# Performance work log

Hardware: AMD Instinct MI355X
Metric: run time of the kernel (lower is better)

The kernel has to match this reference:

```python
import jax, jax.numpy as jnp
import numpy as np
from jax import lax

# Mamba2 config (matches init_kwargs + mamba_ssm defaults)
B_SZ, SEQ = 8, 2048
D_MODEL, D_STATE, EXPAND, HEADDIM = 1024, 128, 2, 64
D_INNER = EXPAND * D_MODEL            # 2048
NHEADS = D_INNER // HEADDIM           # 32
NGROUPS, D_CONV, CHUNK = 1, 4, 128
CONV_DIM = D_INNER + 2 * NGROUPS * D_STATE
D_IN_PROJ = 2 * D_INNER + 2 * NGROUPS * D_STATE + NHEADS
VAR_NUM, EPS = 3, 1e-5


def setup_inputs() -> dict:
    key = jax.random.key(0)
    ks = jax.random.split(key, 10)
    return {
        "embed_data": jax.random.normal(ks[0], (B_SZ, SEQ, D_MODEL), jnp.float32),
        "in_proj_w": jax.random.normal(ks[1], (D_IN_PROJ, D_MODEL), jnp.float32) * 0.02,
        "conv_w": jax.random.normal(ks[2], (CONV_DIM, D_CONV), jnp.float32) * 0.2,
        "conv_b": jnp.zeros((CONV_DIM,), jnp.float32),
        "dt_bias": jnp.log(jnp.expm1(jax.random.uniform(ks[3], (NHEADS,), jnp.float32, 1e-3, 0.1))),
        "A_log": jnp.log(jax.random.uniform(ks[4], (NHEADS,), jnp.float32, 1.0, 16.0)),
        "D": jnp.ones((NHEADS,), jnp.float32),
        "norm_w": jnp.ones((D_INNER,), jnp.float32),
        "out_proj_w": jax.random.normal(ks[5], (D_MODEL, D_INNER), jnp.float32) * 0.02,
        "dec_w": jax.random.normal(ks[6], (VAR_NUM, D_MODEL), jnp.float32) * 0.02,
        "dec_b": jnp.zeros((VAR_NUM,), jnp.float32),
    }


def _segsum(a):
    # a: (b,h,c,L) -> (b,h,c,L,L) lower-triangular segment sums
    L = a.shape[-1]
    cs = jnp.cumsum(a, -1)
    ss = cs[..., :, None] - cs[..., None, :]
    mask = jnp.tril(jnp.ones((L, L), bool))
    return jnp.where(mask, ss, -jnp.inf)


def _ssd(x, dt, A, Bm, Cm):
    # x:(b,l,h,p) dt:(b,l,h) A:(h,) Bm,Cm:(b,l,n); chunked SSD scan (Mamba2)
    b, l, h, p = x.shape
    n = Bm.shape[-1]
    c = l // CHUNK
    xc = x.reshape(b, c, CHUNK, h, p)
    dtc = dt.reshape(b, c, CHUNK, h)
    Bc = Bm.reshape(b, c, CHUNK, n)
    Cc = Cm.reshape(b, c, CHUNK, n)
    ac = (dt * A).reshape(b, c, CHUNK, h).transpose(0, 3, 1, 2)  # (b,h,c,L)
    acs = jnp.cumsum(ac, -1)
    Lmat = jnp.exp(_segsum(ac))                                   # (b,h,c,L,L)
    xdt = xc * dtc[..., None]
    # intra-chunk (diagonal block) outputs
    CB = jnp.einsum('bcln,bcsn->bcls', Cc, Bc)
    Y_diag = jnp.einsum('bcls,bhcls,bcshp->bclhp', CB, Lmat, xdt)
    # per-chunk final states
    decay_states = jnp.exp(acs[..., -1:] - acs)                   # (b,h,c,L)
    states = jnp.einsum('bcln,bhcl,bclhp->bchpn', Bc, decay_states, xdt)
    chunk_decay = jnp.exp(acs[..., -1])                           # (b,h,c)
    def step(carry, inp):
        st, dec = inp
        return carry * dec[..., None, None] + st, carry
    _, states_in = lax.scan(step, jnp.zeros((b, h, p, n), x.dtype),
                            (jnp.moveaxis(states, 1, 0), jnp.moveaxis(chunk_decay, 2, 0)))
    states_in = jnp.moveaxis(states_in, 0, 1)                     # (b,c,h,p,n)
    # inter-chunk (off-diagonal) contribution
    Y_off = jnp.einsum('bcln,bchpn,bhcl->bclhp', Cc, states_in, jnp.exp(acs))
    return (Y_diag + Y_off).reshape(b, l, h, p)


def reference(embed_data, in_proj_w, conv_w, conv_b, dt_bias, A_log, D, norm_w, out_proj_w, dec_w, dec_b):
    b, l, _ = embed_data.shape
    zxbcdt = embed_data @ in_proj_w.T                             # (b,l,D_IN_PROJ)
    z = zxbcdt[..., :D_INNER]
    xBC = zxbcdt[..., D_INNER:D_INNER + CONV_DIM]
    dt = jax.nn.softplus(zxbcdt[..., D_INNER + CONV_DIM:] + dt_bias)  # (b,l,h)
    # causal depthwise conv1d + SiLU
    xt = lax.conv_general_dilated(xBC.transpose(0, 2, 1), conv_w[:, None, :], (1,),
                                  [(D_CONV - 1, 0)], feature_group_count=CONV_DIM,
                                  dimension_numbers=('NCH', 'OIH', 'NCH'))
    xBC = jax.nn.silu(xt.transpose(0, 2, 1) + conv_b)
    x = xBC[..., :D_INNER].reshape(b, l, NHEADS, HEADDIM)
    Bm = xBC[..., D_INNER:D_INNER + D_STATE]
    Cm = xBC[..., D_INNER + D_STATE:]
    A = -jnp.exp(A_log)
    y = _ssd(x, dt, A, Bm, Cm) + D[None, None, :, None] * x
    # gated RMSNorm
    y = y.reshape(b, l, D_INNER) * jax.nn.silu(z)
    y = y * lax.rsqrt(jnp.mean(y * y, -1, keepdims=True) + EPS) * norm_w
    hidden = y @ out_proj_w.T
    pred = hidden @ dec_w.T + dec_b
    return pred, hidden
```

## Files before the change

kernel.cpp:

```cpp
#include <hip/hip_runtime.h>
#include <cstdint>

#define DEVI __device__ __forceinline__

typedef unsigned short u16;
typedef unsigned int u32;
typedef __attribute__((ext_vector_type(4))) float f32x4;
typedef __attribute__((ext_vector_type(8))) u16 u16x8;
typedef __attribute__((ext_vector_type(4))) u16 u16x4;
typedef __attribute__((ext_vector_type(8))) __bf16 bf16x8;

#define SEQL 2048
#define NBATCH 8
#define MROWS (NBATCH*SEQL)
#define DMODEL 1024
#define DINNER 2048
#define NHEADS 32
#define HEADD 64
#define DSTATE 128
#define CONVD 2304
#define NPROJ 4384
#define NPROJP 4608
#define CHUNKL 128
#define NCHUNK 16
#define PADC 136

DEVI float bf2f(u16 v){ u32 u = ((u32)v)<<16; return __builtin_bit_cast(float,u); }
DEVI u16 f2bf(float f){ u32 u = __builtin_bit_cast(u32,f); u32 r = (u + 0x7fffu + ((u>>16)&1u))>>16; return (u16)r; }

DEVI void gld_lds16(const void* g, void* lds){
  __builtin_amdgcn_global_load_lds(
    (const __attribute__((address_space(1))) void*)(uintptr_t)g,
    (__attribute__((address_space(3))) void*)(u32)(uintptr_t)lds, 16, 0, 0);
}

DEVI f32x4 MFMA(u16x8 a, u16x8 b, f32x4 c){
  return __builtin_amdgcn_mfma_f32_16x16x32_bf16(
      __builtin_bit_cast(bf16x8,a), __builtin_bit_cast(bf16x8,b), c, 0,0,0);
}

__global__ void k_sentinel(float* o){ o[0] = 12345.0f; }

__global__ __launch_bounds__(256) void k_cvt(const float* __restrict__ src, u16* __restrict__ dst, long n, long ntot){
  long idx = ((long)blockIdx.x*256 + threadIdx.x)*4;
  if (idx >= ntot) return;
  u16x4 o;
  if (idx < n){
    f32x4 v = *(const f32x4*)(src+idx);
    o[0]=f2bf(v[0]); o[1]=f2bf(v[1]); o[2]=f2bf(v[2]); o[3]=f2bf(v[3]);
  } else { o[0]=0; o[1]=0; o[2]=0; o[3]=0; }
  *(u16x4*)(dst+idx) = o;
}

#define STG(mat, h, ts) do { \
    const int d_ = (ts) & 1; \
    const size_t ko_ = (size_t)(((ts) < NT) ? (ts) : (NT-1)) * 64; \
    gld_lds16(sbase[mat][h][0] + ko_, (char*)lds + (mat)*65536 + (d_*2+(h))*16384 + tid*16); \
    gld_lds16(sbase[mat][h][1] + ko_, (char*)lds + (mat)*65536 + (d_*2+(h))*16384 + 8192 + tid*16); \
  } while(0)

#define LDA8(AF, d_, qm) { \
    _Pragma("unroll") for (int mf=0; mf<4; mf++) \
    _Pragma("unroll") for (int ks=0; ks<2; ks++) \
      AF[mf][ks] = *(const u16x8*)(lds + (size_t)((d_)*2+wm)*8192 + ((qm)*64+mf*16+lidx)*64 + ((ks*4+krow)^(lidx&7))*8); }

#define LDB4(BF, d_, qn) { \
    _Pragma("unroll") for (int nf=0; nf<2; nf++) \
    _Pragma("unroll") for (int ks=0; ks<2; ks++) \
      BF[nf][ks] = *(const u16x8*)(lds + 32768 + (size_t)((d_)*2+(wn>>1))*8192 + ((wn&1)*64+(qn)*32+nf*16+lidx)*64 + ((ks*4+krow)^(lidx&7))*8); }

#define MMAQ(QM, QN, AF, BF) { \
    _Pragma("unroll") for (int mf=0; mf<4; mf++) \
    _Pragma("unroll") for (int nf=0; nf<2; nf++) \
    _Pragma("unroll") for (int ks=0; ks<2; ks++) \
      acc[(QM)*4+mf][(QN)*2+nf] = MFMA(AF[mf][ks], BF[nf][ks], acc[(QM)*4+mf][(QN)*2+nf]); }

#define BAR1 __builtin_amdgcn_sched_barrier(0); __builtin_amdgcn_s_barrier(); \
    asm volatile("s_waitcnt lgkmcnt(0)" ::: "memory"); __builtin_amdgcn_sched_barrier(0); \
    __builtin_amdgcn_s_setprio(1);
#define BAR2 __builtin_amdgcn_s_setprio(0); __builtin_amdgcn_sched_barrier(0); \
    __builtin_amdgcn_s_barrier(); __builtin_amdgcn_sched_barrier(0);

template<int MODE>
__global__ __launch_bounds__(512, 2) void k_gemm8(const u16* __restrict__ A, const u16* __restrict__ Bt,
    const int K, const int Ndim, float* __restrict__ outF,
    u16* __restrict__ z_out, u16* __restrict__ xbc_out, float* __restrict__ dtraw_out)
{
  extern __shared__ u16 lds[];
  const int NT = K >> 6;
  const int tid = threadIdx.x;
  const int lane = tid & 63, wid = tid >> 6;
  const int wm = wid >> 2, wn = wid & 3;
  const int lidx = lane & 15, krow = lane >> 4;
  const int nwg = gridDim.x * gridDim.y;
  const int orig = blockIdx.y * gridDim.x + blockIdx.x;
  const int swz = (orig & 7) * (nwg >> 3) + (orig >> 3);
  const int m0 = (swz % gridDim.x) * 256;
  const int n0 = (swz / gridDim.x) * 256;

  f32x4 acc[8][4];
  const f32x4 zf = {0.f,0.f,0.f,0.f};
  #pragma unroll
  for (int i=0;i<8;i++)
    #pragma unroll
    for (int j=0;j<4;j++) acc[i][j] = zf;

  const int r0 = tid >> 3;
  const int gsw = ((tid & 7) ^ (r0 & 7)) * 8;
  const u16* sbase[2][2][2];
  #pragma unroll
  for (int h=0; h<2; h++)
    #pragma unroll
    for (int L=0; L<2; L++){
      sbase[0][h][L] = A  + (size_t)(m0 + h*128 + L*64 + r0)*K + gsw;
      sbase[1][h][L] = Bt + (size_t)(n0 + h*128 + L*64 + r0)*K + gsw;
    }

  STG(0,0,0); STG(0,1,0); STG(1,0,0); STG(1,1,0);
  asm volatile("s_waitcnt vmcnt(4)" ::: "memory");
  STG(0,0,1); STG(0,1,1); STG(1,0,1);
  asm volatile("s_waitcnt vmcnt(6)" ::: "memory");
  __builtin_amdgcn_sched_barrier(0);
  __builtin_amdgcn_s_barrier();
  __builtin_amdgcn_sched_barrier(0);

  u16x8 af[4][2], bf0[2][2], bf1[2][2];
  for (int t = 0; t < NT; t += 2){
    LDA8(af, 0, 0); LDB4(bf0, 0, 0); STG(1,1,t+1);
    BAR1; MMAQ(0,0,af,bf0); BAR2;
    LDB4(bf1, 0, 1);
    BAR1; MMAQ(0,1,af,bf1); BAR2;
    LDA8(af, 0, 1); STG(1,0,t+2);
    BAR1; MMAQ(1,1,af,bf1); BAR2;
    STG(0,0,t+2); STG(0,1,t+2);
    asm volatile("s_waitcnt vmcnt(6)" ::: "memory");
    BAR1; MMAQ(1,0,af,bf0); BAR2;
    LDA8(af, 1, 0); LDB4(bf0, 1, 0); STG(1,1,t+2);
    BAR1; MMAQ(0,0,af,bf0); BAR2;
    LDB4(bf1, 1, 1);
    BAR1; MMAQ(0,1,af,bf1); BAR2;
    LDA8(af, 1, 1); STG(1,0,t+3);
    BAR1; MMAQ(1,1,af,bf1); BAR2;
    STG(0,0,t+3); STG(0,1,t+3);
    asm volatile("s_waitcnt vmcnt(6)" ::: "memory");
    BAR1; MMAQ(1,0,af,bf0); BAR2;
  }
  asm volatile("s_waitcnt vmcnt(0)" ::: "memory");

  #pragma unroll
  for (int im=0; im<8; im++)
    #pragma unroll
    for (int in=0; in<4; in++)
      #pragma unroll
      for (int r=0; r<4; r++){
        int gm = m0 + wm*128 + im*16 + krow*4 + r;
        int gn = n0 + wn*64 + in*16 + lidx;
        float v = acc[im][in][r];
        if (MODE==0){
          outF[(long)gm*Ndim + gn] = v;
        } else {
          if (gn < DINNER) z_out[(long)gm*DINNER + gn] = f2bf(v);
          else if (gn < DINNER+CONVD) xbc_out[(long)gm*CONVD + (gn-DINNER)] = f2bf(v);
          else if (gn < NPROJ) dtraw_out[(long)gm*NHEADS + (gn-DINNER-CONVD)] = v;
        }
      }
}

__global__ __launch_bounds__(128) void k_dtprep(const float* __restrict__ dtraw, const float* __restrict__ dt_bias,
    const float* __restrict__ A_log, float* __restrict__ dt_t, float* __restrict__ acs_t)
{
  int b = blockIdx.x >> 9;
  int h = (blockIdx.x >> 4) & 31;
  int c = blockIdx.x & 15;
  int l = threadIdx.x;
  int gl = c*128 + l;
  float raw = dtraw[((long)(b*SEQL + gl))*NHEADS + h] + dt_bias[h];
  float dt = (raw > 20.f) ? raw : log1pf(expf(raw));
  float A = -expf(A_log[h]);
  float ac = dt*A;
  __shared__ float ss[128];
  ss[l] = ac; __syncthreads();
  for (int o=1;o<128;o<<=1){
    float v = (l>=o)? ss[l-o] : 0.f;
    __syncthreads();
    ss[l] += v;
    __syncthreads();
  }
  float acs = ss[l];
  dt_t[((long)(b*NHEADS+h))*SEQL + gl] = dt;
  acs_t[((long)(b*NHEADS+h))*SEQL + gl] = acs;
}

__global__ __launch_bounds__(256) void k_conv(const u16* __restrict__ xbc, const float* __restrict__ conv_w,
    const float* __restrict__ conv_b, const float* __restrict__ dt_t,
    u16* __restrict__ xdtT, u16* __restrict__ BTt, u16* __restrict__ CTt)
{
  __shared__ u16 sm[131*64];
  int idx = blockIdx.x;
  int b = idx / 576; int rem = idx % 576; int cbk = rem >> 4; int lb = rem & 15;
  int ch0 = cbk*64, l0 = lb*128;
  for (int g = threadIdx.x; g < 131*8; g += 256){
    int r = g >> 3, cg = g & 7;
    int gl = l0 - 3 + r;
    u16x8 v;
    if (gl >= 0) v = *(const u16x8*)(xbc + ((long)(b*SEQL+gl))*CONVD + ch0 + cg*8);
    else { v[0]=0;v[1]=0;v[2]=0;v[3]=0;v[4]=0;v[5]=0;v[6]=0;v[7]=0; }
    *(u16x8*)(&sm[r*64 + cg*8]) = v;
  }
  __syncthreads();
  int ci = threadIdx.x & 63, g4 = threadIdx.x >> 6;
  int chg = ch0 + ci;
  f32x4 wv = *(const f32x4*)(conv_w + chg*4);
  float bia = conv_b[chg];
  bool isX = chg < DINNER;
  int h = chg >> 6; if (h > 31) h = 31;
  int p = chg & 63;
  const float* dtrow = dt_t + ((long)(b*NHEADS+h))*SEQL + l0 + g4*32;
  u16x8 ov[4];
  #pragma unroll
  for (int i=0;i<32;i++){
    int lr = g4*32 + i;
    float a = bia + wv[0]*bf2f(sm[(lr+0)*64+ci]) + wv[1]*bf2f(sm[(lr+1)*64+ci])
                  + wv[2]*bf2f(sm[(lr+2)*64+ci]) + wv[3]*bf2f(sm[(lr+3)*64+ci]);
    float s = a / (1.f + __expf(-a));
    if (isX) s *= dtrow[i];
    ov[i>>3][i&7] = f2bf(s);
  }
  u16* dst;
  if (isX)                      dst = xdtT + (((long)(b*NHEADS+h))*HEADD + p)*SEQL + l0 + g4*32;
  else if (chg < DINNER+DSTATE) dst = BTt + ((long)(b*DSTATE + (chg-DINNER)))*SEQL + l0 + g4*32;
  else                          dst = CTt + ((long)(b*DSTATE + (chg-DINNER-DSTATE)))*SEQL + l0 + g4*32;
  #pragma unroll
  for (int q=0;q<4;q++) *(u16x8*)(dst + q*8) = ov[q];
}

__global__ __launch_bounds__(256) void k_cb(const u16* __restrict__ BTt, const u16* __restrict__ CTt,
      u16* __restrict__ CBm, u16* __restrict__ Cn)
{
  __shared__ u16 Cl[128*136];
  __shared__ u16 Bl[128*136];
  int b = blockIdx.x >> 4, c = blockIdx.x & 15;
  for (int g = threadIdx.x; g < 2048; g += 256){
    int n = g >> 4, lg = g & 15;
    u16x8 vc = *(const u16x8*)(CTt + ((long)(b*DSTATE+n))*SEQL + c*CHUNKL + lg*8);
    u16x8 vb = *(const u16x8*)(BTt + ((long)(b*DSTATE+n))*SEQL + c*CHUNKL + lg*8);
    #pragma unroll
    for (int j=0;j<8;j++){
      Cl[(lg*8+j)*136 + n] = vc[j];
      Bl[(lg*8+j)*136 + n] = vb[j];
    }
  }
  __syncthreads();
  const int tid = threadIdx.x;
  const int lane = tid & 63, wid = tid >> 6;
  const int wr = wid & 1, wc2 = wid >> 1;
  const int lidx = lane & 15, krow = lane >> 4;
  const f32x4 zf = {0.f,0.f,0.f,0.f};
  f32x4 acc[4][4];
  #pragma unroll
  for (int i=0;i<4;i++)
    #pragma unroll
    for (int j=0;j<4;j++) acc[i][j] = zf;
  #pragma unroll
  for (int k0=0;k0<128;k0+=32){
    u16x8 af[4], bfv[4];
    #pragma unroll
    for (int i=0;i<4;i++){
      af[i]  = *(const u16x8*)(&Cl[(wr*64+i*16+lidx)*136 + k0 + krow*8]);
      bfv[i] = *(const u16x8*)(&Bl[(wc2*64+i*16+lidx)*136 + k0 + krow*8]);
    }
    #pragma unroll
    for (int i=0;i<4;i++)
      #pragma unroll
      for (int j=0;j<4;j++)
        acc[i][j] = MFMA(af[i], bfv[j], acc[i][j]);
  }
  long base = ((long)(b*16+c))*128*128;
  #pragma unroll
  for (int i=0;i<4;i++)
    #pragma unroll
    for (int j=0;j<4;j++)
      #pragma unroll
      for (int r=0;r<4;r++){
        int l = wr*64+i*16+krow*4+r;
        int s = wc2*64+j*16+lidx;
        CBm[base + (long)l*128 + s] = f2bf(acc[i][j][r]);
      }
  for (int g = tid; g < 2048; g += 256){
    int l = g >> 4, ng = g & 15;
    u16x8 o;
    #pragma unroll
    for (int j=0;j<8;j++) o[j] = Cl[l*136 + ng*8 + j];
    *(u16x8*)(Cn + ((long)(b*SEQL + c*CHUNKL + l))*DSTATE + ng*8) = o;
  }
}

__global__ __launch_bounds__(256) void k_ssd(
    const u16* __restrict__ Cng, const u16* __restrict__ BTt, const u16* __restrict__ xdtT,
    const u16* __restrict__ CBm, const float* __restrict__ acs_t, const float* __restrict__ dt_t,
    const float* __restrict__ Dparam, u16* __restrict__ y)
{
  __shared__ u16 Cs[128*PADC];
  __shared__ u16 Bs[128*PADC];
  __shared__ u16 Ps[128*PADC];
  __shared__ u16 Xs[64*PADC];
  __shared__ float carry[64*132];
  __shared__ float acs_s[128], eacs_s[128], dec_s[128], dtr_s[128];
  const int bh = blockIdx.x;
  const int b = bh >> 5, h = bh & 31;
  const int tid = threadIdx.x, lane = tid & 63, wid = tid >> 6;
  const int lidx = lane & 15, krow = lane >> 4;
  const int wl = wid & 1, wp = wid >> 1;
  const int wps = wid & 1, wns = wid >> 1;
  for (int i = tid; i < 64*132; i += 256) carry[i] = 0.f;
  const float Dh = Dparam[h];
  const float* acs_g = acs_t + (long)bh*SEQL;
  const float* dt_g = dt_t + (long)bh*SEQL;
  const u16* X_g = xdtT + (long)bh*HEADD*SEQL;
  const u16* B_g = BTt + (long)b*DSTATE*SEQL;
  const u16* C_g = Cng + (long)b*SEQL*DSTATE;
  const u16* CB_g = CBm + (long)b*NCHUNK*CHUNKL*CHUNKL;
  const f32x4 zf = {0.f,0.f,0.f,0.f};
  for (int c=0;c<NCHUNK;c++){
    __syncthreads();
    if (tid < 128){ acs_s[tid] = acs_g[c*128+tid]; dtr_s[tid] = dt_g[c*128+tid]; }
    __syncthreads();
    if (tid < 128){ float a = acs_s[tid]; eacs_s[tid] = __expf(a); dec_s[tid] = __expf(acs_s[127]-a); }
    __syncthreads();
    for (int g = tid; g < 2048; g += 256){
      int l = g >> 4, cb = g & 15;
      u16x8 v = *(const u16x8*)(C_g + ((long)(c*128+l))*DSTATE + cb*8);
      float e = eacs_s[l];
      u16x8 o;
      #pragma unroll
      for (int j=0;j<8;j++) o[j] = f2bf(bf2f(v[j])*e);
      *(u16x8*)(&Cs[l*PADC + cb*8]) = o;
    }
    for (int g = tid; g < 2048; g += 256){
      int n = g >> 4, lg = g & 15;
      u16x8 v = *(const u16x8*)(B_g + (long)n*SEQL + c*128 + lg*8);
      u16x8 o;
      #pragma unroll
      for (int j=0;j<8;j++) o[j] = f2bf(bf2f(v[j])*dec_s[lg*8+j]);
      *(u16x8*)(&Bs[n*PADC + lg*8]) = o;
    }
    for (int g = tid; g < 1024; g += 256){
      int p = g >> 4, lg = g & 15;
      *(u16x8*)(&Xs[p*PADC + lg*8]) = *(const u16x8*)(X_g + (long)p*SEQL + c*128 + lg*8);
    }
    {
      int l = tid >> 1, s0 = (tid & 1)*64;
      float al = acs_s[l];
      #pragma unroll
      for (int q=0;q<8;q++){
        u16x8 v = *(const u16x8*)(CB_g + ((long)(c*128+l))*CHUNKL + s0 + q*8);
        u16x8 o;
        #pragma unroll
        for (int j=0;j<8;j++){
          int s = s0 + q*8 + j;
          float pv = (s <= l) ? bf2f(v[j]) * __expf(al - acs_s[s]) : 0.f;
          o[j] = f2bf(pv);
        }
        *(u16x8*)(&Ps[l*PADC + s0 + q*8]) = o;
      }
    }
    __syncthreads();
    f32x4 accY[4][2];
    f32x4 accS[2][4];
    #pragma unroll
    for (int i=0;i<4;i++){ accY[i][0]=zf; accY[i][1]=zf; }
    #pragma unroll
    for (int i=0;i<2;i++){ accS[i][0]=zf; accS[i][1]=zf; accS[i][2]=zf; accS[i][3]=zf; }
    #pragma unroll
    for (int k0=0;k0<128;k0+=32){
      u16x8 af[4], bfv[2];
      #pragma unroll
      for (int i=0;i<4;i++) af[i] = *(const u16x8*)(&Cs[(wl*64+i*16+lidx)*PADC + k0 + krow*8]);
      #pragma unroll
      for (int j=0;j<2;j++){
        const float* cp = &carry[(wp*32+j*16+lidx)*132 + k0 + krow*8];
        f32x4 c0 = *(const f32x4*)cp;
        f32x4 c1 = *(const f32x4*)(cp+4);
        u16x8 o;
        o[0]=f2bf(c0[0]); o[1]=f2bf(c0[1]); o[2]=f2bf(c0[2]); o[3]=f2bf(c0[3]);
        o[4]=f2bf(c1[0]); o[5]=f2bf(c1[1]); o[6]=f2bf(c1[2]); o[7]=f2bf(c1[3]);
        bfv[j] = o;
      }
      #pragma unroll
      for (int i=0;i<4;i++)
        #pragma unroll
        for (int j=0;j<2;j++)
          accY[i][j] = MFMA(af[i], bfv[j], accY[i][j]);
    }
    #pragma unroll
    for (int k0=0;k0<128;k0+=32){
      u16x8 af[4], bfv[2];
      #pragma unroll
      for (int i=0;i<4;i++) af[i] = *(const u16x8*)(&Ps[(wl*64+i*16+lidx)*PADC + k0 + krow*8]);
      #pragma unroll
      for (int j=0;j<2;j++) bfv[j] = *(const u16x8*)(&Xs[(wp*32+j*16+lidx)*PADC + k0 + krow*8]);
      #pragma unroll
      for (int i=0;i<4;i++)
        #pragma unroll
        for (int j=0;j<2;j++)
          accY[i][j] = MFMA(af[i], bfv[j], accY[i][j]);
    }
    #pragma unroll
    for (int k0=0;k0<128;k0+=32){
      u16x8 as2[2], bs2[4];
      #pragma unroll
      for (int i=0;i<2;i++) as2[i] = *(const u16x8*)(&Xs[(wps*32+i*16+lidx)*PADC + k0 + krow*8]);
      #pragma unroll
      for (int j=0;j<4;j++) bs2[j] = *(const u16x8*)(&Bs[(wns*64+j*16+lidx)*PADC + k0 + krow*8]);
      #pragma unroll
      for (int i=0;i<2;i++)
        #pragma unroll
        for (int j=0;j<4;j++)
          accS[i][j] = MFMA(as2[i], bs2[j], accS[i][j]);
    }
    __syncthreads();
    float cd = __expf(acs_s[127]);
    #pragma unroll
    for (int i=0;i<2;i++)
      #pragma unroll
      for (int j=0;j<4;j++)
        #pragma unroll
        for (int r=0;r<4;r++){
          int p = wps*32 + i*16 + krow*4 + r;
          int n = wns*64 + j*16 + lidx;
          carry[p*132+n] = carry[p*132+n]*cd + accS[i][j][r];
        }
    #pragma unroll
    for (int i=0;i<4;i++)
      #pragma unroll
      for (int j=0;j<2;j++)
        #pragma unroll
        for (int r=0;r<4;r++){
          int l = wl*64 + i*16 + krow*4 + r;
          int p = wp*32 + j*16 + lidx;
          float xv = bf2f(Xs[p*PADC + l]) / dtr_s[l];
          float val = accY[i][j][r] + Dh*xv;
          y[((long)(b*SEQL + c*128 + l))*DINNER + h*HEADD + p] = f2bf(val);
        }
  }
}

__global__ __launch_bounds__(256) void k_gate(const u16* __restrict__ y, const u16* __restrict__ z,
    const float* __restrict__ norm_w, u16* __restrict__ out)
{
  long row = blockIdx.x;
  const u16* yr = y + row*DINNER;
  const u16* zr = z + row*DINNER;
  int t = threadIdx.x;
  u16x8 yy = *(const u16x8*)(yr + t*8);
  u16x8 zz = *(const u16x8*)(zr + t*8);
  float g[8]; float ss = 0.f;
  #pragma unroll
  for (int j=0;j<8;j++){
    float zfv = bf2f(zz[j]);
    float sg = zfv / (1.f + __expf(-zfv));
    float gv = bf2f(yy[j]) * sg;
    g[j] = gv; ss += gv*gv;
  }
  #pragma unroll
  for (int o=32;o>0;o>>=1) ss += __shfl_down(ss, o);
  __shared__ float part[4];
  int lane = t & 63, wid = t>>6;
  if (lane==0) part[wid] = ss;
  __syncthreads();
  float tot = part[0]+part[1]+part[2]+part[3];
  float inv = rsqrtf(tot*(1.f/DINNER) + 1e-5f);
  u16x8 o;
  #pragma unroll
  for (int j=0;j<8;j++) o[j] = f2bf(g[j]*inv*norm_w[t*8+j]);
  *(u16x8*)(out + row*DINNER + t*8) = o;
}

__global__ __launch_bounds__(256) void k_pred(const float* __restrict__ hid, const float* __restrict__ dec_w,
    const float* __restrict__ dec_b, float* __restrict__ pred)
{
  int t = threadIdx.x;
  long row = (long)blockIdx.x*8 + (t>>5);
  int lk = t & 31;
  const float* hr = hid + row*DMODEL;
  float a0=0.f,a1=0.f,a2=0.f;
  #pragma unroll
  for (int i=0;i<8;i++){
    f32x4 hv = *(const f32x4*)(hr + lk*4 + i*128);
    f32x4 w0 = *(const f32x4*)(dec_w + 0*DMODEL + lk*4 + i*128);
    f32x4 w1 = *(const f32x4*)(dec_w + 1*DMODEL + lk*4 + i*128);
    f32x4 w2 = *(const f32x4*)(dec_w + 2*DMODEL + lk*4 + i*128);
    a0 += hv[0]*w0[0]+hv[1]*w0[1]+hv[2]*w0[2]+hv[3]*w0[3];
    a1 += hv[0]*w1[0]+hv[1]*w1[1]+hv[2]*w1[2]+hv[3]*w1[3];
    a2 += hv[0]*w2[0]+hv[1]*w2[1]+hv[2]*w2[2]+hv[3]*w2[3];
  }
  #pragma unroll
  for (int o=16;o>0;o>>=1){
    a0 += __shfl_down(a0,o,32); a1 += __shfl_down(a1,o,32); a2 += __shfl_down(a2,o,32);
  }
  if (lk==0){
    pred[row*3+0] = a0 + dec_b[0];
    pred[row*3+1] = a1 + dec_b[1];
    pred[row*3+2] = a2 + dec_b[2];
  }
}

extern "C" void kernel_launch(void* const* d_in, const int* in_sizes, int n_in,
                              void* d_out, int out_size, void* d_ws, size_t ws_size,
                              hipStream_t stream)
{
  const float* embed      = (const float*)d_in[0];
  const float* in_proj_w  = (const float*)d_in[1];
  const float* conv_w     = (const float*)d_in[2];
  const float* conv_b     = (const float*)d_in[3];
  const float* dt_bias    = (const float*)d_in[4];
  const float* A_log      = (const float*)d_in[5];
  const float* Dp         = (const float*)d_in[6];
  const float* norm_w     = (const float*)d_in[7];
  const float* out_proj_w = (const float*)d_in[8];
  const float* dec_w      = (const float*)d_in[9];
  const float* dec_b      = (const float*)d_in[10];

  char* ws = (char*)d_ws;
  size_t off = 0;
  auto alloc = [&](size_t bytes)->void*{ void* p = ws + off; off += (bytes + 255) & ~(size_t)255; return p; };

  u16* xbc = (u16*)alloc((size_t)MROWS*CONVD*2);
  u16* yb  = xbc;
  u16* R2  = (u16*)alloc((size_t)MROWS*DINNER*2);
  u16* Ebf = R2;
  u16* W1  = R2 + (size_t)MROWS*DMODEL;
  u16* xdtT  = R2;
  u16* ynorm = R2;
  float* dtraw = (float*)alloc((size_t)MROWS*NHEADS*4);
  float* dt_t  = (float*)alloc((size_t)NBATCH*NHEADS*SEQL*4);
  float* acs   = (float*)alloc((size_t)NBATCH*NHEADS*SEQL*4);
  u16* BTt   = (u16*)alloc((size_t)NBATCH*DSTATE*SEQL*2);
  u16* CTt   = (u16*)alloc((size_t)NBATCH*DSTATE*SEQL*2);
  u16* Cn    = (u16*)alloc((size_t)NBATCH*SEQL*DSTATE*2);
  u16* CBm   = (u16*)alloc((size_t)NBATCH*NCHUNK*CHUNKL*CHUNKL*2);
  u16* W2    = (u16*)alloc((size_t)DMODEL*DINNER*2);

  if (off > ws_size){
    k_sentinel<<<1,1,0,stream>>>((float*)d_out);
    return;
  }

  float* pred   = (float*)d_out;
  float* hidden = (float*)d_out + (size_t)MROWS*3;
  u16* zb = (u16*)hidden;

  hipFuncSetAttribute((const void*)k_gemm8<1>, hipFuncAttributeMaxDynamicSharedMemorySize, 131072);
  hipFuncSetAttribute((const void*)k_gemm8<0>, hipFuncAttributeMaxDynamicSharedMemorySize, 131072);

  k_cvt<<<16384,256,0,stream>>>(embed, Ebf, (long)MROWS*DMODEL, (long)MROWS*DMODEL);
  k_cvt<<<4608,256,0,stream>>>(in_proj_w, W1, (long)NPROJ*DMODEL, (long)NPROJP*DMODEL);
  k_cvt<<<2048,256,0,stream>>>(out_proj_w, W2, (long)DMODEL*DINNER, (long)DMODEL*DINNER);
  {
    dim3 g1(64, NPROJP/256);
    k_gemm8<1><<<g1,512,131072,stream>>>(Ebf, W1, DMODEL, 0, nullptr, zb, xbc, dtraw);
  }
  k_dtprep<<<4096,128,0,stream>>>(dtraw, dt_bias, A_log, dt_t, acs);
  k_conv<<<4608,256,0,stream>>>(xbc, conv_w, conv_b, dt_t, xdtT, BTt, CTt);
  k_cb<<<128,256,0,stream>>>(BTt, CTt, CBm, Cn);
  k_ssd<<<256,256,0,stream>>>(Cn, BTt, xdtT, CBm, acs, dt_t, Dp, yb);
  k_gate<<<16384,256,0,stream>>>(yb, zb, norm_w, ynorm);
  {
    dim3 g2(64, DMODEL/256);
    k_gemm8<0><<<g2,512,131072,stream>>>(ynorm, W2, DINNER, DMODEL, hidden, nullptr, nullptr, nullptr);
  }
  k_pred<<<2048,256,0,stream>>>(hidden, dec_w, dec_b, pred);
}
```

Baseline: 648.0 us.

## Split sequential SSD kernel into parallel chunk-state, scan, and output kernels

Replaces the single k_ssd kernel, which runs 256 blocks (one per batch-head) serially over 16 chunks, with three kernels. k_par computes each chunk's local state in parallel (4096 blocks), k_scan does a cheap inter-chunk recurrence on the states, and k_yoff computes the intra-chunk plus state-contribution outputs in parallel. The aim is to fix the low occupancy of the 256-block sequential scan on a GPU with many CUs. In exchange it writes and reads a 64MB bf16 state buffer, rounds carried states to bf16, and adds launches. The old path is kept as a fallback when the workspace is too small.

After: 553.1 us. 1.17x faster.

```diff
diff --git a/kernel.cpp b/kernel.cpp
--- a/kernel.cpp
+++ b/kernel.cpp
@@ -293,6 +293,205 @@
     for (int j=0;j<8;j++) o[j] = Cl[l*136 + ng*8 + j];
     *(u16x8*)(Cn + ((long)(b*SEQL + c*CHUNKL + l))*DSTATE + ng*8) = o;
   }
+}
+
+__global__ __launch_bounds__(256) void k_par(
+    const u16* __restrict__ BTt, const u16* __restrict__ xdtT,
+    const float* __restrict__ acs_t, u16* __restrict__ states)
+{
+  __shared__ u16 Bs[128*PADC];
+  __shared__ u16 Xs[64*PADC];
+  __shared__ float acs_s[128], dec_s[128];
+  const int idx = blockIdx.x;
+  const int c = idx & 15, bh = idx >> 4, b = bh >> 5;
+  const int tid = threadIdx.x, lane = tid & 63, wid = tid >> 6;
+  const int lidx = lane & 15, krow = lane >> 4;
+  const int wps = wid & 1, wns = wid >> 1;
+  const float* acs_g = acs_t + (long)bh*SEQL + c*128;
+  const u16* X_g = xdtT + (long)bh*HEADD*SEQL + c*128;
+  const u16* B_g = BTt + (long)b*DSTATE*SEQL + c*128;
+  if (tid < 128) acs_s[tid] = acs_g[tid];
+  __syncthreads();
+  if (tid < 128) dec_s[tid] = __expf(acs_s[127] - acs_s[tid]);
+  __syncthreads();
+  for (int g = tid; g < 2048; g += 256){
+    int n = g >> 4, lg = g & 15;
+    u16x8 v = *(const u16x8*)(B_g + (long)n*SEQL + lg*8);
+    u16x8 o;
+    #pragma unroll
+    for (int j=0;j<8;j++) o[j] = f2bf(bf2f(v[j])*dec_s[lg*8+j]);
+    *(u16x8*)(&Bs[n*PADC + lg*8]) = o;
+  }
+  for (int g = tid; g < 1024; g += 256){
+    int p = g >> 4, lg = g & 15;
+    *(u16x8*)(&Xs[p*PADC + lg*8]) = *(const u16x8*)(X_g + (long)p*SEQL + lg*8);
+  }
+  __syncthreads();
+  const f32x4 zf = {0.f,0.f,0.f,0.f};
+  f32x4 accS[2][4];
+  #pragma unroll
+  for (int i=0;i<2;i++){ accS[i][0]=zf; accS[i][1]=zf; accS[i][2]=zf; accS[i][3]=zf; }
+  #pragma unroll
+  for (int k0=0;k0<128;k0+=32){
+    u16x8 as2[2], bs2[4];
+    #pragma unroll
+    for (int i=0;i<2;i++) as2[i] = *(const u16x8*)(&Xs[(wps*32+i*16+lidx)*PADC + k0 + krow*8]);
+    #pragma unroll
+    for (int j=0;j<4;j++) bs2[j] = *(const u16x8*)(&Bs[(wns*64+j*16+lidx)*PADC + k0 + krow*8]);
+    #pragma unroll
+    for (int i=0;i<2;i++)
+      #pragma unroll
+      for (int j=0;j<4;j++)
+        accS[i][j] = MFMA(as2[i], bs2[j], accS[i][j]);
+  }
+  u16* Sg = states + (long)idx*8192;
+  #pragma unroll
+  for (int i=0;i<2;i++)
+    #pragma unroll
+    for (int j=0;j<4;j++)
+      #pragma unroll
+      for (int r=0;r<4;r++){
+        int p = wps*32 + i*16 + krow*4 + r;
+        int n = wns*64 + j*16 + lidx;
+        Sg[p*128 + n] = f2bf(accS[i][j][r]);
+      }
+}
+
+__global__ __launch_bounds__(256) void k_scan(u16* __restrict__ states, const float* __restrict__ acs_t)
+{
+  long gid = (long)blockIdx.x*256 + threadIdx.x;
+  int bh = (int)(gid >> 11);
+  int q = (int)(gid & 2047);
+  __shared__ float cds[16];
+  if (threadIdx.x < 16) cds[threadIdx.x] = __expf(acs_t[(long)bh*SEQL + threadIdx.x*128 + 127]);
+  __syncthreads();
+  u16* p = states + (long)bh*NCHUNK*8192 + q*4;
+  u16x4 sv[16];
+  #pragma unroll
+  for (int c=0;c<16;c++) sv[c] = *(const u16x4*)(p + c*8192);
+  float c0=0.f,c1=0.f,c2=0.f,c3=0.f;
+  #pragma unroll
+  for (int c=0;c<16;c++){
+    u16x4 o; o[0]=f2bf(c0); o[1]=f2bf(c1); o[2]=f2bf(c2); o[3]=f2bf(c3);
+    *(u16x4*)(p + c*8192) = o;
+    float cd = cds[c];
+    c0 = c0*cd + bf2f(sv[c][0]);
+    c1 = c1*cd + bf2f(sv[c][1]);
+    c2 = c2*cd + bf2f(sv[c][2]);
+    c3 = c3*cd + bf2f(sv[c][3]);
+  }
+}
+
+__global__ __launch_bounds__(256) void k_yoff(
+    const u16* __restrict__ Cng, const u16* __restrict__ xdtT, const u16* __restrict__ CBm,
+    const u16* __restrict__ SI, const float* __restrict__ acs_t, const float* __restrict__ dt_t,
+    const float* __restrict__ Dparam, u16* __restrict__ y)
+{
+  __shared__ u16 Ts[128*PADC];
+  __shared__ u16 Us[64*PADC];
+  __shared__ float acs_s[128], dtr_s[128], eacs_s[128];
+  const int idx = blockIdx.x;
+  const int c = idx & 15, bh = idx >> 4, b = bh >> 5, h = bh & 31;
+  const int tid = threadIdx.x, lane = tid & 63, wid = tid >> 6;
+  const int lidx = lane & 15, krow = lane >> 4;
+  const int wl = wid & 1, wp = wid >> 1;
+  const float Dh = Dparam[h];
+  const float* acs_g = acs_t + (long)bh*SEQL + c*128;
+  const float* dt_g  = dt_t  + (long)bh*SEQL + c*128;
+  const u16* X_g = xdtT + (long)bh*HEADD*SEQL + c*128;
+  const u16* C_g = Cng + ((long)(b*SEQL + c*128))*DSTATE;
+  const u16* CB_g = CBm + ((long)(b*NCHUNK + c))*CHUNKL*CHUNKL;
+  const u16* SI_g = SI + (long)idx*8192;
+  if (tid < 128){ acs_s[tid] = acs_g[tid]; dtr_s[tid] = dt_g[tid]; }
+  __syncthreads();
+  if (tid < 128) eacs_s[tid] = __expf(acs_s[tid]);
+  __syncthreads();
+  {
+    int l = tid >> 1, s0 = (tid & 1)*64;
+    float al = acs_s[l];
+    #pragma unroll
+    for (int qq=0;qq<8;qq++){
+      u16x8 v = *(const u16x8*)(CB_g + (long)l*CHUNKL + s0 + qq*8);
+      u16x8 o;
+      #pragma unroll
+      for (int j=0;j<8;j++){
+        int s = s0 + qq*8 + j;
+        float pv = (s <= l) ? bf2f(v[j]) * __expf(al - acs_s[s]) : 0.f;
+        o[j] = f2bf(pv);
+      }
+      *(u16x8*)(&Ts[l*PADC + s0 + qq*8]) = o;
+    }
+  }
+  for (int g = tid; g < 1024; g += 256){
+    int p = g >> 4, lg = g & 15;
+    *(u16x8*)(&Us[p*PADC + lg*8]) = *(const u16x8*)(X_g + (long)p*SEQL + lg*8);
+  }
+  __syncthreads();
+  const f32x4 zf = {0.f,0.f,0.f,0.f};
+  f32x4 accY[4][2];
+  #pragma unroll
+  for (int i=0;i<4;i++){ accY[i][0]=zf; accY[i][1]=zf; }
+  #pragma unroll
+  for (int k0=0;k0<128;k0+=32){
+    u16x8 af[4], bfv[2];
+    #pragma unroll
+    for (int i=0;i<4;i++) af[i] = *(const u16x8*)(&Ts[(wl*64+i*16+lidx)*PADC + k0 + krow*8]);
+    #pragma unroll
+    for (int j=0;j<2;j++) bfv[j] = *(const u16x8*)(&Us[(wp*32+j*16+lidx)*PADC + k0 + krow*8]);
+    #pragma unroll
+    for (int i=0;i<4;i++)
+      #pragma unroll
+      for (int j=0;j<2;j++)
+        accY[i][j] = MFMA(af[i], bfv[j], accY[i][j]);
+  }
+  #pragma unroll
+  for (int i=0;i<4;i++)
+    #pragma unroll
+    for (int j=0;j<2;j++)
+      #pragma unroll
+      for (int r=0;r<4;r++){
+        int l = wl*64 + i*16 + krow*4 + r;
+        int p = wp*32 + j*16 + lidx;
+        accY[i][j][r] += Dh * bf2f(Us[p*PADC + l]) / dtr_s[l];
+      }
+  __syncthreads();
+  for (int g = tid; g < 2048; g += 256){
+    int l = g >> 4, cb = g & 15;
+    u16x8 v = *(const u16x8*)(C_g + (long)l*DSTATE + cb*8);
+    float e = eacs_s[l];
+    u16x8 o;
+    #pragma unroll
+    for (int j=0;j<8;j++) o[j] = f2bf(bf2f(v[j])*e);
+    *(u16x8*)(&Ts[l*PADC + cb*8]) = o;
+  }
+  for (int g = tid; g < 1024; g += 256){
+    int p = g >> 4, lg = g & 15;
+    *(u16x8*)(&Us[p*PADC + lg*8]) = *(const u16x8*)(SI_g + p*128 + lg*8);
+  }
+  __syncthreads();
+  #pragma unroll
+  for (int k0=0;k0<128;k0+=32){
+    u16x8 af[4], bfv[2];
+    #pragma unroll
+    for (int i=0;i<4;i++) af[i] = *(const u16x8*)(&Ts[(wl*64+i*16+lidx)*PADC + k0 + krow*8]);
+    #pragma unroll
+    for (int j=0;j<2;j++) bfv[j] = *(const u16x8*)(&Us[(wp*32+j*16+lidx)*PADC + k0 + krow*8]);
+    #pragma unroll
+    for (int i=0;i<4;i++)
+      #pragma unroll
+      for (int j=0;j<2;j++)
+        accY[i][j] = MFMA(af[i], bfv[j], accY[i][j]);
+  }
+  #pragma unroll
+  for (int i=0;i<4;i++)
+    #pragma unroll
+    for (int j=0;j<2;j++)
+      #pragma unroll
+      for (int r=0;r<4;r++){
+        int l = wl*64 + i*16 + krow*4 + r;
+        int p = wp*32 + j*16 + lidx;
+        y[((long)(b*SEQL + c*128 + l))*DINNER + h*HEADD + p] = f2bf(accY[i][j][r]);
+      }
 }
 
 __global__ __launch_bounds__(256) void k_ssd(
@@ -541,7 +740,11 @@
   u16* CBm   = (u16*)alloc((size_t)NBATCH*NCHUNK*CHUNKL*CHUNKL*2);
   u16* W2    = (u16*)alloc((size_t)DMODEL*DINNER*2);
 
-  if (off > ws_size){
+  size_t off_base = off;
+  u16* S = (u16*)alloc((size_t)NBATCH*NHEADS*NCHUNK*HEADD*DSTATE*2);
+  bool use_par = (off <= ws_size);
+
+  if (off_base > ws_size){
     k_sentinel<<<1,1,0,stream>>>((float*)d_out);
     return;
   }
@@ -563,7 +766,13 @@
   k_dtprep<<<4096,128,0,stream>>>(dtraw, dt_bias, A_log, dt_t, acs);
   k_conv<<<4608,256,0,stream>>>(xbc, conv_w, conv_b, dt_t, xdtT, BTt, CTt);
   k_cb<<<128,256,0,stream>>>(BTt, CTt, CBm, Cn);
-  k_ssd<<<256,256,0,stream>>>(Cn, BTt, xdtT, CBm, acs, dt_t, Dp, yb);
+  if (use_par){
+    k_par<<<4096,256,0,stream>>>(BTt, xdtT, acs, S);
+    k_scan<<<2048,256,0,stream>>>(S, acs);
+    k_yoff<<<4096,256,0,stream>>>(Cn, xdtT, CBm, S, acs, dt_t, Dp, yb);
+  } else {
+    k_ssd<<<256,256,0,stream>>>(Cn, BTt, xdtT, CBm, acs, dt_t, Dp, yb);
+  }
   k_gate<<<16384,256,0,stream>>>(yb, zb, norm_w, ynorm);
   {
     dim3 g2(64, DMODEL/256);
```
